# Kernel tuning notes

Hardware: AMD Instinct MI355X
Metric: run time of the kernel (lower is better)

## Reference

```python
import jax, jax.numpy as jnp
import numpy as np

N, E, IN, H, O, D = 1024, 65536, 768, 512, 256, 5
THRESH = 0.5
SAVE_W = [float(np.exp(0.0)), float(np.exp(-1.0)), float(np.exp(-2.0))]  # exp(-layers_pos)


def _gcn_conv(x, ei, ew, W, b):
    """PyG GCNConv: x@W, add self-loops (weight 1), symmetric degree norm, scatter-add."""
    n = x.shape[0]
    h = x @ W                                   # [n, out]
    loop = jnp.arange(n)
    src = jnp.concatenate([ei[0], loop])
    dst = jnp.concatenate([ei[1], loop])
    w = jnp.concatenate([ew, jnp.ones((n,), h.dtype)])
    deg = jax.ops.segment_sum(w, dst, num_segments=n)
    dinv = jnp.where(deg > 0, deg ** -0.5, 0.0)
    coef = dinv[src] * w * dinv[dst]
    return jax.ops.segment_sum(coef[:, None] * h[src], dst, num_segments=n) + b


def _spectral_flags(X):
    """Cosine-similarity graph -> unnormalized Laplacian -> eigengap-based class ids (int)."""
    Xn = X / (jnp.linalg.norm(X, axis=1, keepdims=True) + 1e-8)
    S = Xn @ Xn.T                               # [N, N]
    Lap = jnp.diag(S.sum(1)) - S
    ev = jax.lax.stop_gradient(jnp.linalg.eigvalsh(Lap))  # discrete downstream -> no grad
    order = jnp.argsort(ev)
    sv = ev[order]
    newc = (jnp.diff(sv) > THRESH).astype(jnp.int32)
    cls_sorted = jnp.concatenate([jnp.zeros((1,), jnp.int32), jnp.cumsum(newc)])
    return jnp.zeros((X.shape[0],), jnp.int32).at[order].set(cls_sorted)


def _class_avg(flags, X):
    """Per-class mean feature, gathered back to every node."""
    n = X.shape[0]
    sums = jax.ops.segment_sum(X, flags, num_segments=n)
    cnt = jax.ops.segment_sum(jnp.ones((n,), X.dtype), flags, num_segments=n)
    avg = sums / jnp.clip(cnt, 1.0)[:, None]
    return avg[flags]


def setup_inputs() -> dict:
    key = jax.random.key(0)
    ks = jax.random.split(key, 32)
    f32 = jnp.float32

    def p(k, shape, fan_in):
        return jax.random.normal(k, shape, f32) * (fan_in ** -0.5)

    inp = {}
    for i in range(5):
        inp[f'dim{i + 1}'] = jax.random.normal(ks[i], (N, IN), f32)
    inp['edge_indices'] = jax.random.randint(ks[5], (D, 2, E), 0, N)
    inp['edge_weights'] = jax.random.uniform(ks[6], (D, E), f32, 0.1, 1.0)
    inp['non_zero'] = jax.random.uniform(ks[7], (N,), f32, 1.0, 5.0)
    inp['gcn_w1'] = p(ks[8], (D, H, H), H)
    inp['gcn_b1'] = p(ks[9], (D, H), H)
    inp['gcn_w2'] = p(ks[10], (D, O, O), O)
    inp['gcn_b2'] = p(ks[11], (D, O), O)
    inp['gcn_w3'] = p(ks[12], (D, O, O), O)
    inp['gcn_b3'] = p(ks[13], (D, O), O)
    inp['gcn_wb'] = p(ks[14], (D, O, O), O)   # beh_conv1 (the only beh conv actually called)
    inp['gcn_bb'] = p(ks[15], (D, O), O)
    inp['w_pre1'] = p(ks[16], (IN, H), IN)
    inp['b_pre1'] = p(ks[17], (H,), IN)
    inp['w_pre2'] = p(ks[18], (H, O), H)
    inp['b_pre2'] = p(ks[19], (O,), H)
    inp['w_pre3'] = p(ks[20], (O, O), O)
    inp['b_pre3'] = p(ks[21], (O,), O)
    inp['w_beh1'] = p(ks[22], (O, O), O)
    inp['b_beh1'] = p(ks[23], (O,), O)
    inp['w_beh2'] = p(ks[24], (O, O), O)
    inp['b_beh2'] = p(ks[25], (O,), O)
    inp['w_beh3'] = p(ks[26], (O, O), O)
    inp['b_beh3'] = p(ks[27], (O,), O)
    inp['dim_weights'] = jnp.ones((D,), f32) + 0.1 * jax.random.normal(ks[28], (D,), f32)
    inp['k_save'] = jnp.asarray(0.5, f32)
    return inp


def reference(dim1, dim2, dim3, dim4, dim5, edge_indices, edge_weights, non_zero,
              gcn_w1, gcn_b1, gcn_w2, gcn_b2, gcn_w3, gcn_b3, gcn_wb, gcn_bb,
              w_pre1, b_pre1, w_pre2, b_pre2, w_pre3, b_pre3,
              w_beh1, b_beh1, w_beh2, b_beh2, w_beh3, b_beh3,
              dim_weights, k_save):
    dims = jnp.stack([dim1, dim2, dim3, dim4, dim5])      # [D, N, IN]
    dw = dim_weights / dim_weights.sum()
    gcn = jax.vmap(_gcn_conv)

    def pre_layer(x, Wl, bl, Wg, bg, save_w):
        lin = jnp.einsum('dni,io->dno', x, Wl) + bl       # shared Linear over all dims
        outs = gcn(lin, edge_indices, edge_weights, Wg, bg)
        fused = jnp.einsum('d,dnc->nc', dw, outs)         # weighted dimension fusion
        mg = lin + (save_w * fused / non_zero[:, None])[None]
        return jax.nn.relu(lin + mg)                      # relu(lin + (lin + upd))

    L1 = pre_layer(dims, w_pre1, b_pre1, gcn_w1, gcn_b1, SAVE_W[0])
    L2 = pre_layer(L1, w_pre2, b_pre2, gcn_w2, gcn_b2, SAVE_W[1])
    L3 = pre_layer(L2, w_pre3, b_pre3, gcn_w3, gcn_b3, SAVE_W[2])

    def beh_layer(g_in, fir, Wl, bl):
        g = gcn(g_in, edge_indices, edge_weights, gcn_wb, gcn_bb)  # always beh_conv1
        flags = jax.vmap(_spectral_flags)(g)
        avg = jax.vmap(_class_avg)(flags, g)
        lin = jnp.einsum('dni,io->dno', avg, Wl) + bl
        fea = fir + k_save * lin
        return g, jax.nn.relu(fir + fea)

    g4, L4 = beh_layer(L3, L3, w_beh1, b_beh1)
    g5, L5 = beh_layer(g4, L4, w_beh2, b_beh2)
    g6, L6 = beh_layer(g5, L5, w_beh3, b_beh3)
    return L6.sum(axis=0) + 1e-8                          # [N, O]
```

## Files before the change

### kernel.cpp

```cpp
#include <hip/hip_runtime.h>
#include <math.h>


#define NNODE 1024
#define NEDGE 65536
#define NDIM  5
#define TN    1024
#define TDW   48

struct P5 { const float* p[5]; };

__device__ __forceinline__ float wave_red_sum(float v) {
#pragma unroll
  for (int o = 32; o; o >>= 1) v += __shfl_xor(v, o);
  return v;
}

__global__ __launch_bounds__(256) void ws_fail_kernel(float* __restrict__ out, float val) {
  out[(size_t)blockIdx.x * 256 + threadIdx.x] = val;
}

__global__ __launch_bounds__(256) void count_edges_kernel(const int* __restrict__ eidx,
                                                          int* __restrict__ cnt) {
  long i = (long)blockIdx.x * 256 + threadIdx.x;
  if (i >= (long)NDIM * NEDGE) return;
  int d = (int)(i / NEDGE), e = (int)(i % NEDGE);
  int dst = eidx[(long)d * 2 * NEDGE + NEDGE + e];
  atomicAdd(&cnt[d * NNODE + dst], 1);
}

__global__ __launch_bounds__(1024) void scan_kernel(const int* __restrict__ cnt,
                                                    int* __restrict__ rowptr,
                                                    int* __restrict__ fillpos) {
  int d = blockIdx.x, i = threadIdx.x;
  __shared__ int s[1024];
  int c = cnt[d * NNODE + i];
  s[i] = c;
  __syncthreads();
  for (int off = 1; off < 1024; off <<= 1) {
    int t = (i >= off) ? s[i - off] : 0;
    __syncthreads();
    s[i] += t;
    __syncthreads();
  }
  int excl = s[i] - c;
  rowptr[d * (NNODE + 1) + i] = excl;
  fillpos[d * NNODE + i] = excl;
  if (i == 1023) rowptr[d * (NNODE + 1) + NNODE] = s[i];
}

__global__ __launch_bounds__(256) void csr_fill_kernel(const int* __restrict__ eidx,
                                                       int* __restrict__ fillpos,
                                                       int* __restrict__ csr) {
  long i = (long)blockIdx.x * 256 + threadIdx.x;
  if (i >= (long)NDIM * NEDGE) return;
  int d = (int)(i / NEDGE), e = (int)(i % NEDGE);
  int dst = eidx[(long)d * 2 * NEDGE + NEDGE + e];
  int pos = atomicAdd(&fillpos[d * NNODE + dst], 1);
  csr[(long)d * NEDGE + pos] = e;
}

__global__ __launch_bounds__(256) void csr_sort_kernel(const int* __restrict__ rowptr,
                                                       int* __restrict__ csr) {
  int idx = blockIdx.x * 256 + threadIdx.x;
  if (idx >= NDIM * NNODE) return;
  int d = idx >> 10, n = idx & 1023;
  int rs = rowptr[d * (NNODE + 1) + n], re = rowptr[d * (NNODE + 1) + n + 1];
  int* a = csr + (long)d * NEDGE;
  for (int i = rs + 1; i < re; ++i) {
    int key = a[i]; int j = i - 1;
    while (j >= rs && a[j] > key) { a[j + 1] = a[j]; --j; }
    a[j + 1] = key;
  }
}

__global__ __launch_bounds__(256) void deg_kernel(const int* __restrict__ rowptr,
                                                  const int* __restrict__ csr,
                                                  const float* __restrict__ ew,
                                                  float* __restrict__ dinv,
                                                  float* __restrict__ selfc) {
  int idx = blockIdx.x * 256 + threadIdx.x;
  if (idx >= NDIM * NNODE) return;
  int d = idx >> 10, n = idx & 1023;
  int rs = rowptr[d * (NNODE + 1) + n], re = rowptr[d * (NNODE + 1) + n + 1];
  const float* ewd = ew + (long)d * NEDGE;
  const int* csrd = csr + (long)d * NEDGE;
  float deg = 1.0f;
  for (int t = rs; t < re; ++t) deg += ewd[csrd[t]];
  float di = 1.0f / sqrtf(deg);
  dinv[idx] = di;
  selfc[idx] = di * di;
}

__global__ __launch_bounds__(256) void coef_kernel(const int* __restrict__ eidx,
                                                   const float* __restrict__ ew,
                                                   const float* __restrict__ dinv,
                                                   float* __restrict__ coef) {
  long i = (long)blockIdx.x * 256 + threadIdx.x;
  if (i >= (long)NDIM * NEDGE) return;
  int d = (int)(i / NEDGE), e = (int)(i % NEDGE);
  int s = eidx[(long)d * 2 * NEDGE + e];
  int t = eidx[(long)d * 2 * NEDGE + NEDGE + e];
  coef[i] = dinv[d * NNODE + s] * ew[i] * dinv[d * NNODE + t];
}

__global__ __launch_bounds__(256) void gemm_nn(P5 Ap, const float* __restrict__ B, long Bstr,
                                               const float* __restrict__ bias,
                                               float* __restrict__ C, long Cstr,
                                               int Nn, int K) {
  int z = blockIdx.z;
  const float* A = Ap.p[z];
  const float* Bz = B + (size_t)z * Bstr;
  float* Cz = C + (size_t)z * Cstr;
  __shared__ float As[16][65], Bs[16][65];
  int bx = blockIdx.x * 64, by = blockIdx.y * 64;
  int tid = threadIdx.x, tx = tid & 15, ty = tid >> 4;
  float acc[4][4] = {};
  for (int k0 = 0; k0 < K; k0 += 16) {
    {
      int r = tid >> 2, kk = (tid & 3) * 4;
      float4 v = *(const float4*)(A + (size_t)(by + r) * K + k0 + kk);
      As[kk + 0][r] = v.x; As[kk + 1][r] = v.y; As[kk + 2][r] = v.z; As[kk + 3][r] = v.w;
    }
    {
      int kk = tid >> 4, c4 = (tid & 15) * 4;
      float4 v = *(const float4*)(Bz + (size_t)(k0 + kk) * Nn + bx + c4);
      Bs[kk][c4 + 0] = v.x; Bs[kk][c4 + 1] = v.y; Bs[kk][c4 + 2] = v.z; Bs[kk][c4 + 3] = v.w;
    }
    __syncthreads();
#pragma unroll
    for (int kk = 0; kk < 16; ++kk) {
      float a[4], b[4];
#pragma unroll
      for (int u = 0; u < 4; ++u) { a[u] = As[kk][ty * 4 + u]; b[u] = Bs[kk][tx * 4 + u]; }
#pragma unroll
      for (int ii = 0; ii < 4; ++ii)
#pragma unroll
        for (int jj = 0; jj < 4; ++jj) acc[ii][jj] += a[ii] * b[jj];
    }
    __syncthreads();
  }
#pragma unroll
  for (int ii = 0; ii < 4; ++ii)
#pragma unroll
    for (int jj = 0; jj < 4; ++jj) {
      int gj = bx + tx * 4 + jj;
      float v = acc[ii][jj];
      if (bias) v += bias[gj];
      Cz[(size_t)(by + ty * 4 + ii) * Nn + gj] = v;
    }
}

__global__ __launch_bounds__(256) void gemm_nt_lap(const float* __restrict__ Xn,
                                                   const float* __restrict__ svec,
                                                   float* __restrict__ Lap) {
  int z = blockIdx.z;
  const float* X = Xn + (size_t)z * NNODE * 256;
  float* C = Lap + (size_t)z * NNODE * NNODE;
  __shared__ float As[16][65], Bs[16][65];
  int bx = blockIdx.x * 64, by = blockIdx.y * 64;
  int tid = threadIdx.x, tx = tid & 15, ty = tid >> 4;
  float acc[4][4] = {};
  for (int k0 = 0; k0 < 256; k0 += 16) {
    int r = tid >> 2, kk = (tid & 3) * 4;
    float4 va = *(const float4*)(X + (size_t)(by + r) * 256 + k0 + kk);
    As[kk + 0][r] = va.x; As[kk + 1][r] = va.y; As[kk + 2][r] = va.z; As[kk + 3][r] = va.w;
    float4 vb4 = *(const float4*)(X + (size_t)(bx + r) * 256 + k0 + kk);
    Bs[kk + 0][r] = vb4.x; Bs[kk + 1][r] = vb4.y; Bs[kk + 2][r] = vb4.z; Bs[kk + 3][r] = vb4.w;
    __syncthreads();
#pragma unroll
    for (int kk2 = 0; kk2 < 16; ++kk2) {
      float a[4], b[4];
#pragma unroll
      for (int u = 0; u < 4; ++u) { a[u] = As[kk2][ty * 4 + u]; b[u] = Bs[kk2][tx * 4 + u]; }
#pragma unroll
      for (int ii = 0; ii < 4; ++ii)
#pragma unroll
        for (int jj = 0; jj < 4; ++jj) acc[ii][jj] += a[ii] * b[jj];
    }
    __syncthreads();
  }
#pragma unroll
  for (int ii = 0; ii < 4; ++ii)
#pragma unroll
    for (int jj = 0; jj < 4; ++jj) {
      int gi = by + ty * 4 + ii, gj = bx + tx * 4 + jj;
      float v = -acc[ii][jj];
      if (gi == gj) v += svec[z * NNODE + gi];
      C[(size_t)gi * NNODE + gj] = v;
    }
}

__global__ __launch_bounds__(256) void gcn_gather(const float* __restrict__ h,
                                                  const int* __restrict__ eidx,
                                                  const int* __restrict__ csr,
                                                  const int* __restrict__ rowptr,
                                                  const float* __restrict__ coef,
                                                  const float* __restrict__ selfc,
                                                  const float* __restrict__ bg,
                                                  float* __restrict__ outp, int C) {
  int n = blockIdx.x, d = blockIdx.y;
  const float* hd = h + (size_t)d * NNODE * C;
  float* od = outp + (size_t)d * NNODE * C;
  const int* srcA = eidx + (size_t)d * 2 * NEDGE;
  const float* coefd = coef + (size_t)d * NEDGE;
  const int* csrd = csr + (size_t)d * NEDGE;
  int rs = rowptr[d * (NNODE + 1) + n], re = rowptr[d * (NNODE + 1) + n + 1];
  float sc = selfc[d * NNODE + n];
  for (int c = threadIdx.x; c < C; c += 256) {
    float acc = sc * hd[(size_t)n * C + c] + bg[d * C + c];
    for (int idx = rs; idx < re; ++idx) {
      int e = csrd[idx];
      acc += coefd[e] * hd[(size_t)srcA[e] * C + c];
    }
    od[(size_t)n * C + c] = acc;
  }
}

__global__ __launch_bounds__(256) void pre_fuse(const float* __restrict__ lin,
                                                const float* __restrict__ outs,
                                                const float* __restrict__ nz,
                                                const float* __restrict__ dimw,
                                                float saveW, float* __restrict__ Lout, int C) {
  size_t i = (size_t)blockIdx.x * 256 + threadIdx.x;
  int n = (int)(i / C);
  float s0 = dimw[0], s1 = dimw[1], s2 = dimw[2], s3 = dimw[3], s4 = dimw[4];
  float S = s0 + s1 + s2 + s3 + s4;
  size_t st = (size_t)NNODE * C;
  float fused = s0 * outs[i] + s1 * outs[i + st] + s2 * outs[i + 2 * st] +
                s3 * outs[i + 3 * st] + s4 * outs[i + 4 * st];
  float addv = saveW * fused / (S * nz[n]);
#pragma unroll
  for (int d = 0; d < 5; ++d) {
    float l = lin[i + d * st];
    Lout[i + d * st] = fmaxf(2.f * l + addv, 0.f);
  }
}

__global__ __launch_bounds__(256) void rownorm_kernel(const float* __restrict__ g,
                                                      float* __restrict__ Xn) {
  int n = blockIdx.x, d = blockIdx.y, t = threadIdx.x;
  __shared__ float red[4];
  size_t base = ((size_t)d * NNODE + n) * 256;
  float v = g[base + t];
  float sq = wave_red_sum(v * v);
  if ((t & 63) == 0) red[t >> 6] = sq;
  __syncthreads();
  float ss = red[0] + red[1] + red[2] + red[3];
  float inv = 1.f / (sqrtf(ss) + 1e-8f);
  Xn[base + t] = v * inv;
}

__global__ __launch_bounds__(256) void colsum_kernel(const float* __restrict__ Xn,
                                                     float* __restrict__ tcol) {
  int d = blockIdx.y, c = threadIdx.x;
  float acc = 0.f;
  const float* p = Xn + (size_t)d * NNODE * 256 + c;
  for (int i = 0; i < NNODE; ++i) acc += p[(size_t)i * 256];
  tcol[d * 256 + c] = acc;
}

__global__ __launch_bounds__(256) void sdot_kernel(const float* __restrict__ Xn,
                                                   const float* __restrict__ tcol,
                                                   float* __restrict__ svec) {
  int n = blockIdx.x, d = blockIdx.y, t = threadIdx.x;
  __shared__ float red[4];
  size_t base = ((size_t)d * NNODE + n) * 256;
  float v = wave_red_sum(Xn[base + t] * tcol[d * 256 + t]);
  if ((t & 63) == 0) red[t >> 6] = v;
  __syncthreads();
  if (t == 0) svec[d * NNODE + n] = red[0] + red[1] + red[2] + red[3];
}

__global__ __launch_bounds__(256) void col_init_kernel(const float* __restrict__ Lap,
                                                       float* __restrict__ colbufG) {
  int i = blockIdx.x * 256 + threadIdx.x;
  int d = blockIdx.y;
  colbufG[(size_t)d * TN + i] = Lap[(size_t)d * TN * TN + (size_t)i * TN + 0];
}

__global__ __launch_bounds__(256) void tristep(float* __restrict__ Amats,
                                               float* __restrict__ colbufG,
                                               float* __restrict__ prawG,
                                               float* __restrict__ vglobG,
                                               float* __restrict__ tauG,
                                               float* __restrict__ dT,
                                               float* __restrict__ eT,
                                               int k) {
  const int mat = blockIdx.x % NDIM;
  const int wgl = blockIdx.x / NDIM;
  const int WGM = gridDim.x / NDIM;
  const int WPM = WGM * 4;
  const int tid = threadIdx.x;
  const int lane = tid & 63;
  const int wid = tid >> 6;
  const int wv = wgl * 4 + wid;

  float* A = Amats + (size_t)mat * TN * TN;
  const int s0 = k & 1, s1 = (k + 1) & 1;
  const float* colA = colbufG + ((size_t)s0 * NDIM + mat) * TN;
  float* colB = colbufG + ((size_t)s1 * NDIM + mat) * TN;
  const float* prawP = prawG + ((size_t)s1 * NDIM + mat) * TN;
  float* prawC = prawG + ((size_t)s0 * NDIM + mat) * TN;
  const float* vprevG = vglobG + ((size_t)s1 * NDIM + mat) * TN;
  float* vcurG = vglobG + ((size_t)s0 * NDIM + mat) * TN;

  __shared__ float vprev[TN], vcur[TN], wb[TN];
  __shared__ float redA[4], redK[4];

  float tau_prev = (k > 0) ? tauG[s1 * NDIM + mat] : 0.f;

  float kp = 0.f;
  for (int j = k + tid; j < TN; j += 256) {
    float v = (k > 0) ? vprevG[j] : 0.f;
    vprev[j] = v;
    kp += (k > 0) ? v * prawP[j] : 0.f;
  }
  kp = wave_red_sum(kp);
  if (lane == 0) redK[wid] = kp;
  __syncthreads();
  float Kraw = redK[0] + redK[1] + redK[2] + redK[3];
  float c2p = 0.5f * tau_prev * tau_prev * Kraw;
  for (int j = k + tid; j < TN; j += 256)
    wb[j] = (k > 0) ? (tau_prev * prawP[j] - c2p * vprev[j]) : 0.f;
  __syncthreads();

  float wkk = wb[k];
  float vkk = vprev[k];
  float sp = 0.f;
  for (int i = k + 1 + tid; i < TN; i += 256) {
    float c = colA[i] - vprev[i] * wkk - wb[i] * vkk;
    vcur[i] = c;
    sp += c * c;
  }
  sp = wave_red_sum(sp);
  if (lane == 0) redA[wid] = sp;
  __syncthreads();
  float sigma = redA[0] + redA[1] + redA[2] + redA[3];

  if (wgl == 0 && tid == 0)
    dT[mat * TN + k] = A[(size_t)k * TN + k] - 2.f * vkk * wkk;

  float c0 = vcur[k + 1];
  float alpha, tau;
  if (sigma < 1e-30f) { alpha = 0.f; tau = 0.f; }
  else {
    alpha = (c0 >= 0.f) ? -sqrtf(sigma) : sqrtf(sigma);
    tau = 2.f / (2.f * alpha * (alpha - c0));
  }
  __syncthreads();
  if (tid == 0) vcur[k + 1] = c0 - alpha;
  if (wgl == 0 && tid == 0) { eT[mat * TN + k] = alpha; tauG[s0 * NDIM + mat] = tau; }
  __syncthreads();

  if (wgl == 0)
    for (int j = k + 1 + tid; j < TN; j += 256) vcurG[j] = vcur[j];

  int i0 = (k + 1) + ((wv - ((k + 1) % WPM) + WPM) % WPM);
  for (int i = i0; i < TN; i += WPM) {
    float vi = vprev[i];
    float wi = wb[i];
    float* row = A + (size_t)i * TN;
    float dot = 0.f;
    if (k > 0) {
      for (int j = k + 1 + lane; j < TN; j += 64) {
        float a = row[j] - vi * wb[j] - wi * vprev[j];
        row[j] = a;
        dot += a * vcur[j];
        if (j == k + 1) colB[i] = a;
      }
    } else {
      for (int j = 1 + lane; j < TN; j += 64) {
        float a = row[j];
        dot += a * vcur[j];
        if (j == 1) colB[i] = a;
      }
    }
    dot = wave_red_sum(dot);
    if (lane == 0) prawC[i] = dot;
  }
}

__global__ __launch_bounds__(64) void tritail(const float* __restrict__ Amats,
                                              const float* __restrict__ prawG,
                                              const float* __restrict__ vglobG,
                                              const float* __restrict__ tauG,
                                              float* __restrict__ dT,
                                              float* __restrict__ eT) {
  int mat = threadIdx.x;
  if (mat >= NDIM) return;
  const int k = TN - 3;
  const int s0 = k & 1;
  const float* v = vglobG + ((size_t)s0 * NDIM + mat) * TN;
  const float* pr = prawG + ((size_t)s0 * NDIM + mat) * TN;
  float tau = tauG[s0 * NDIM + mat];
  const float* A = Amats + (size_t)mat * TN * TN;
  const int i1 = TN - 2, i2 = TN - 1;
  float v1 = v[i1], v2 = v[i2];
  float Kraw = v1 * pr[i1] + v2 * pr[i2];
  float c2 = 0.5f * tau * tau * Kraw;
  float w1 = tau * pr[i1] - c2 * v1;
  float w2 = tau * pr[i2] - c2 * v2;
  float a11 = A[(size_t)i1 * TN + i1];
  float a21 = A[(size_t)i2 * TN + i1];
  float a22 = A[(size_t)i2 * TN + i2];
  dT[mat * TN + i1] = a11 - 2.f * v1 * w1;
  eT[mat * TN + i1] = a21 - v2 * w1 - w2 * v1;
  dT[mat * TN + i2] = a22 - 2.f * v2 * w2;
}

__global__ __launch_bounds__(256) void bisect_kernel(const float* __restrict__ dT,
                                                     const float* __restrict__ eT,
                                                     float* __restrict__ ev) {
  int mat = blockIdx.y;
  int i = blockIdx.x * 256 + threadIdx.x;
  __shared__ float ds[TN], es[TN];
  __shared__ float redmn[4], redmx[4];
  for (int t = threadIdx.x; t < TN; t += 256) {
    ds[t] = dT[mat * TN + t];
    es[t] = (t < TN - 1) ? eT[mat * TN + t] : 0.f;
  }
  __syncthreads();
  float mn = 1e30f, mx = -1e30f;
  for (int t = threadIdx.x; t < TN; t += 256) {
    float ep = (t > 0) ? fabsf(es[t - 1]) : 0.f;
    float r = ep + fabsf(es[t]);
    mn = fminf(mn, ds[t] - r);
    mx = fmaxf(mx, ds[t] + r);
  }
#pragma unroll
  for (int o = 32; o; o >>= 1) {
    mn = fminf(mn, __shfl_xor(mn, o));
    mx = fmaxf(mx, __shfl_xor(mx, o));
  }
  if ((threadIdx.x & 63) == 0) { redmn[threadIdx.x >> 6] = mn; redmx[threadIdx.x >> 6] = mx; }
  __syncthreads();
  mn = fminf(fminf(redmn[0], redmn[1]), fminf(redmn[2], redmn[3]));
  mx = fmaxf(fmaxf(redmx[0], redmx[1]), fmaxf(redmx[2], redmx[3]));
  float pad = 1e-3f + 1e-6f * fmaxf(fabsf(mn), fabsf(mx));
  float lo = mn - pad, hi = mx + pad;
  const float PIV = 1e-12f;
  for (int it = 0; it < 40; ++it) {
    float x = 0.5f * (lo + hi);
    if (!(x > lo && x < hi)) break;
    float q = ds[0] - x;
    if (fabsf(q) < PIV) q = -PIV;
    int cntv = (q < 0.f) ? 1 : 0;
    for (int t = 1; t < TN; ++t) {
      float e = es[t - 1];
      q = (ds[t] - x) - __fdividef(e * e, q);
      if (fabsf(q) < PIV) q = -PIV;
      cntv += (q < 0.f) ? 1 : 0;
    }
    if (cntv <= i) lo = x; else hi = x;
  }
  ev[mat * TN + i] = 0.5f * (lo + hi);
}

__global__ __launch_bounds__(1024) void flags_kernel(const float* __restrict__ ev,
                                                     int* __restrict__ flags,
                                                     int* __restrict__ startI,
                                                     int* __restrict__ ncls) {
  int d = blockIdx.x, i = threadIdx.x;
  __shared__ int s[1024];
  float evi = ev[d * TN + i];
  int g = 0;
  if (i < TN - 1) g = ((ev[d * TN + i + 1] - evi) > 0.5f) ? 1 : 0;
  s[i] = g;
  __syncthreads();
  for (int off = 1; off < 1024; off <<= 1) {
    int t = (i >= off) ? s[i - off] : 0;
    __syncthreads();
    s[i] += t;
    __syncthreads();
  }
  int fl = s[i] - g;
  flags[d * TN + i] = fl;
  if (i == 0) startI[d * (TN + 1)] = 0;
  if (i < TN - 1 && g) startI[d * (TN + 1) + fl + 1] = i + 1;
  if (i == TN - 1) { ncls[d] = fl + 1; startI[d * (TN + 1) + fl + 1] = TN; }
}

__global__ __launch_bounds__(256) void class_avg_kernel(const float* __restrict__ g,
                                                        const int* __restrict__ startI,
                                                        const int* __restrict__ ncls,
                                                        float* __restrict__ avg) {
  int c = blockIdx.x, d = blockIdx.y, t = threadIdx.x;
  size_t base = (size_t)d * NNODE * 256;
  float* o = avg + base + (size_t)c * 256 + t;
  if (c >= ncls[d]) { *o = 0.f; return; }
  int rs = startI[d * (NNODE + 1) + c], re = startI[d * (NNODE + 1) + c + 1];
  float acc = 0.f;
  for (int r = rs; r < re; ++r) acc += g[base + (size_t)r * 256 + t];
  *o = acc / (float)(re - rs);
}

__global__ __launch_bounds__(256) void beh_out_kernel(const float* __restrict__ fir,
                                                      const float* __restrict__ linB,
                                                      const int* __restrict__ flags,
                                                      const float* __restrict__ ksave,
                                                      float* __restrict__ Lout) {
  size_t i = (size_t)blockIdx.x * 256 + threadIdx.x;
  int c = (int)(i & 255);
  int n = (int)((i >> 8) & 1023);
  int d = (int)(i >> 18);
  float k = ksave[0];
  int f = flags[d * NNODE + n];
  float lv = linB[((size_t)d * NNODE + f) * 256 + c];
  Lout[i] = fmaxf(2.f * fir[i] + k * lv, 0.f);
}

__global__ __launch_bounds__(256) void final_sum_kernel(const float* __restrict__ L6,
                                                        float* __restrict__ out) {
  size_t i = (size_t)blockIdx.x * 256 + threadIdx.x;
  size_t st = (size_t)NNODE * 256;
  out[i] = L6[i] + L6[i + st] + L6[i + 2 * st] + L6[i + 3 * st] + L6[i + 4 * st] + 1e-8f;
}

extern "C" void kernel_launch(void* const* d_in, const int* in_sizes, int n_in,
                              void* d_out, int out_size, void* d_ws, size_t ws_size,
                              hipStream_t stream) {
  (void)in_sizes; (void)n_in; (void)out_size;
  const float* dimp[5];
  for (int i = 0; i < 5; ++i) dimp[i] = (const float*)d_in[i];
  const int* eidx = (const int*)d_in[5];
  const float* ew = (const float*)d_in[6];
  const float* nz = (const float*)d_in[7];
  const float* gw1 = (const float*)d_in[8];
  const float* gb1 = (const float*)d_in[9];
  const float* gw2 = (const float*)d_in[10];
  const float* gb2 = (const float*)d_in[11];
  const float* gw3 = (const float*)d_in[12];
  const float* gb3 = (const float*)d_in[13];
  const float* gwb = (const float*)d_in[14];
  const float* gbb = (const float*)d_in[15];
  const float* wp1 = (const float*)d_in[16];
  const float* bp1 = (const float*)d_in[17];
  const float* wp2 = (const float*)d_in[18];
  const float* bp2 = (const float*)d_in[19];
  const float* wp3 = (const float*)d_in[20];
  const float* bp3 = (const float*)d_in[21];
  const float* wb1 = (const float*)d_in[22];
  const float* bb1 = (const float*)d_in[23];
  const float* wb2 = (const float*)d_in[24];
  const float* bb2 = (const float*)d_in[25];
  const float* wb3 = (const float*)d_in[26];
  const float* bb3 = (const float*)d_in[27];
  const float* dimw = (const float*)d_in[28];
  const float* ksave = (const float*)d_in[29];
  float* out = (float*)d_out;

  char* wsb = (char*)d_ws;
  size_t off = 0;
  auto alloc = [&](size_t bytes) -> char* {
    char* p = wsb + off;
    off = (off + bytes + 255) & ~(size_t)255;
    return p;
  };
  float* Lap = (float*)alloc((size_t)NDIM * TN * TN * 4);
  float* lin = Lap;
  float* outs = Lap + (size_t)NDIM * NNODE * 512;
  float* hbuf = (float*)alloc((size_t)NDIM * NNODE * 512 * 4);
  float* L1 = (float*)alloc((size_t)NDIM * NNODE * 512 * 4);
  float* L2 = (float*)alloc((size_t)NDIM * NNODE * 256 * 4);
  float* L3 = (float*)alloc((size_t)NDIM * NNODE * 256 * 4);
  float* gA = (float*)alloc((size_t)NDIM * NNODE * 256 * 4);
  float* gB = (float*)alloc((size_t)NDIM * NNODE * 256 * 4);
  float* dinv = (float*)alloc((size_t)NDIM * NNODE * 4);
  float* selfc = (float*)alloc((size_t)NDIM * NNODE * 4);
  int* cnt = (int*)alloc((size_t)NDIM * NNODE * 4);
  int* rowptr = (int*)alloc((size_t)NDIM * (NNODE + 1) * 4);
  int* fillpos = (int*)alloc((size_t)NDIM * NNODE * 4);
  int* csr = (int*)alloc((size_t)NDIM * NEDGE * 4);
  float* coef = (float*)alloc((size_t)NDIM * NEDGE * 4);
  float* tcol = (float*)alloc((size_t)NDIM * 256 * 4);
  float* svec = (float*)alloc((size_t)NDIM * NNODE * 4);
  float* colbufG = (float*)alloc((size_t)2 * NDIM * TN * 4);
  float* prawG = (float*)alloc((size_t)2 * NDIM * TN * 4);
  float* vglobG = (float*)alloc((size_t)2 * NDIM * TN * 4);
  float* tauG = (float*)alloc((size_t)2 * NDIM * 4);
  float* dT = (float*)alloc((size_t)NDIM * NNODE * 4);
  float* eT = (float*)alloc((size_t)NDIM * NNODE * 4);
  float* ev = (float*)alloc((size_t)NDIM * NNODE * 4);
  int* flags = (int*)alloc((size_t)NDIM * NNODE * 4);
  int* startI = (int*)alloc((size_t)NDIM * (NNODE + 1) * 4);
  int* nclsI = (int*)alloc(256);

  if (off > ws_size) {
    ws_fail_kernel<<<dim3(1024), dim3(256), 0, stream>>>(
        out, 1.0e6f + (float)(ws_size >> 20));
    return;
  }

  float* L4 = L1;
  float* L5 = L2;
  float* L6 = L3;
  float* Xn = hbuf;
  float* avgbuf = outs;
  float* linB = lin;

  hipMemsetAsync(cnt, 0, (size_t)NDIM * NNODE * 4, stream);

  dim3 B256(256);
  count_edges_kernel<<<dim3((NDIM * NEDGE) / 256), B256, 0, stream>>>(eidx, cnt);
  scan_kernel<<<dim3(NDIM), dim3(1024), 0, stream>>>(cnt, rowptr, fillpos);
  csr_fill_kernel<<<dim3((NDIM * NEDGE) / 256), B256, 0, stream>>>(eidx, fillpos, csr);
  csr_sort_kernel<<<dim3(20), B256, 0, stream>>>(rowptr, csr);
  deg_kernel<<<dim3(20), B256, 0, stream>>>(rowptr, csr, ew, dinv, selfc);
  coef_kernel<<<dim3((NDIM * NEDGE) / 256), B256, 0, stream>>>(eidx, ew, dinv, coef);

  auto mk5 = [](const float* base, size_t stride) {
    P5 s;
    for (int z = 0; z < 5; ++z) s.p[z] = base + z * stride;
    return s;
  };

  P5 x1; for (int z = 0; z < 5; ++z) x1.p[z] = dimp[z];
  gemm_nn<<<dim3(8, 16, 5), B256, 0, stream>>>(x1, wp1, 0, bp1, lin, (long)NNODE * 512, 512, 768);
  gemm_nn<<<dim3(8, 16, 5), B256, 0, stream>>>(mk5(lin, (size_t)NNODE * 512), gw1, (long)512 * 512,
                                               nullptr, hbuf, (long)NNODE * 512, 512, 512);
  gcn_gather<<<dim3(NNODE, NDIM), B256, 0, stream>>>(hbuf, eidx, csr, rowptr, coef, selfc, gb1, outs, 512);
  pre_fuse<<<dim3(2048), B256, 0, stream>>>(lin, outs, nz, dimw, 1.0f, L1, 512);

  gemm_nn<<<dim3(4, 16, 5), B256, 0, stream>>>(mk5(L1, (size_t)NNODE * 512), wp2, 0, bp2, lin,
                                               (long)NNODE * 256, 256, 512);
  gemm_nn<<<dim3(4, 16, 5), B256, 0, stream>>>(mk5(lin, (size_t)NNODE * 256), gw2, (long)256 * 256,
                                               nullptr, hbuf, (long)NNODE * 256, 256, 256);
  gcn_gather<<<dim3(NNODE, NDIM), B256, 0, stream>>>(hbuf, eidx, csr, rowptr, coef, selfc, gb2, outs, 256);
  pre_fuse<<<dim3(1024), B256, 0, stream>>>(lin, outs, nz, dimw, 0.36787944117144233f, L2, 256);

  gemm_nn<<<dim3(4, 16, 5), B256, 0, stream>>>(mk5(L2, (size_t)NNODE * 256), wp3, 0, bp3, lin,
                                               (long)NNODE * 256, 256, 256);
  gemm_nn<<<dim3(4, 16, 5), B256, 0, stream>>>(mk5(lin, (size_t)NNODE * 256), gw3, (long)256 * 256,
                                               nullptr, hbuf, (long)NNODE * 256, 256, 256);
  gcn_gather<<<dim3(NNODE, NDIM), B256, 0, stream>>>(hbuf, eidx, csr, rowptr, coef, selfc, gb3, outs, 256);
  pre_fuse<<<dim3(1024), B256, 0, stream>>>(lin, outs, nz, dimw, 0.13533528323661270f, L3, 256);

  auto beh = [&](const float* g_in, const float* fir, const float* Wl, const float* bl,
                 float* g_out, float* Lout) {
    gemm_nn<<<dim3(4, 16, 5), B256, 0, stream>>>(mk5(g_in, (size_t)NNODE * 256), gwb, (long)256 * 256,
                                                 nullptr, hbuf, (long)NNODE * 256, 256, 256);
    gcn_gather<<<dim3(NNODE, NDIM), B256, 0, stream>>>(hbuf, eidx, csr, rowptr, coef, selfc, gbb, g_out, 256);
    rownorm_kernel<<<dim3(NNODE, NDIM), B256, 0, stream>>>(g_out, Xn);
    colsum_kernel<<<dim3(1, NDIM), B256, 0, stream>>>(Xn, tcol);
    sdot_kernel<<<dim3(NNODE, NDIM), B256, 0, stream>>>(Xn, tcol, svec);
    gemm_nt_lap<<<dim3(16, 16, 5), B256, 0, stream>>>(Xn, svec, Lap);
    col_init_kernel<<<dim3(4, NDIM), B256, 0, stream>>>(Lap, colbufG);
    for (int k = 0; k <= TN - 3; ++k)
      tristep<<<dim3(NDIM * TDW), B256, 0, stream>>>(Lap, colbufG, prawG, vglobG, tauG, dT, eT, k);
    tritail<<<dim3(1), dim3(64), 0, stream>>>(Lap, prawG, vglobG, tauG, dT, eT);
    bisect_kernel<<<dim3(4, NDIM), B256, 0, stream>>>(dT, eT, ev);
    flags_kernel<<<dim3(NDIM), dim3(1024), 0, stream>>>(ev, flags, startI, nclsI);
    class_avg_kernel<<<dim3(NNODE, NDIM), B256, 0, stream>>>(g_out, startI, nclsI, avgbuf);
    gemm_nn<<<dim3(4, 16, 5), B256, 0, stream>>>(mk5(avgbuf, (size_t)NNODE * 256), Wl, 0, bl, linB,
                                                 (long)NNODE * 256, 256, 256);
    beh_out_kernel<<<dim3(5120), B256, 0, stream>>>(fir, linB, flags, ksave, Lout);
  };
  beh(L3, L3, wb1, bb1, gA, L4);
  beh(gA, L4, wb2, bb2, gB, L5);
  beh(gB, L5, wb3, bb3, gA, L6);

  final_sum_kernel<<<dim3(1024), B256, 0, stream>>>(L6, out);
}
```

Measured before the change: 44.00 ms.

## Batch all three behaviour-layer eigen tridiagonalizations into one 15-matrix pass

The graph-conv chain for the three behaviour layers does not depend on the layer outputs, so all three conv results are computed first. Their fifteen Laplacians are then tridiagonalized together in a single sequence of ~1022 tristep launches, instead of three sequences over five matrices each. This targets the serial per-step launch overhead that dominates the eigen solve. In exchange it needs a larger workspace, spreads fewer workgroups over each matrix (16 instead of 48), and keeps a fallback to the old path when the workspace is too small.

New measurement: 38.48 ms. -12.5%, faster.

```diff
diff --git a/kernel.cpp b/kernel.cpp
--- a/kernel.cpp
+++ b/kernel.cpp
@@ -6,7 +6,9 @@
 #define NEDGE 65536
 #define NDIM  5
 #define TN    1024
+#define NMATS 15
 #define TDW   48
+#define TDWM  16
 
 struct P5 { const float* p[5]; };
 
@@ -286,10 +288,10 @@
                                                float* __restrict__ tauG,
                                                float* __restrict__ dT,
                                                float* __restrict__ eT,
-                                               int k) {
-  const int mat = blockIdx.x % NDIM;
-  const int wgl = blockIdx.x / NDIM;
-  const int WGM = gridDim.x / NDIM;
+                                               int nm, int k) {
+  const int mat = blockIdx.x % nm;
+  const int wgl = blockIdx.x / nm;
+  const int WGM = gridDim.x / nm;
   const int WPM = WGM * 4;
   const int tid = threadIdx.x;
   const int lane = tid & 63;
@@ -298,17 +300,17 @@
 
   float* A = Amats + (size_t)mat * TN * TN;
   const int s0 = k & 1, s1 = (k + 1) & 1;
-  const float* colA = colbufG + ((size_t)s0 * NDIM + mat) * TN;
-  float* colB = colbufG + ((size_t)s1 * NDIM + mat) * TN;
-  const float* prawP = prawG + ((size_t)s1 * NDIM + mat) * TN;
-  float* prawC = prawG + ((size_t)s0 * NDIM + mat) * TN;
-  const float* vprevG = vglobG + ((size_t)s1 * NDIM + mat) * TN;
-  float* vcurG = vglobG + ((size_t)s0 * NDIM + mat) * TN;
+  const float* colA = colbufG + ((size_t)s0 * nm + mat) * TN;
+  float* colB = colbufG + ((size_t)s1 * nm + mat) * TN;
+  const float* prawP = prawG + ((size_t)s1 * nm + mat) * TN;
+  float* prawC = prawG + ((size_t)s0 * nm + mat) * TN;
+  const float* vprevG = vglobG + ((size_t)s1 * nm + mat) * TN;
+  float* vcurG = vglobG + ((size_t)s0 * nm + mat) * TN;
 
   __shared__ float vprev[TN], vcur[TN], wb[TN];
   __shared__ float redA[4], redK[4];
 
-  float tau_prev = (k > 0) ? tauG[s1 * NDIM + mat] : 0.f;
+  float tau_prev = (k > 0) ? tauG[s1 * nm + mat] : 0.f;
 
   float kp = 0.f;
   for (int j = k + tid; j < TN; j += 256) {
@@ -350,7 +352,7 @@
   }
   __syncthreads();
   if (tid == 0) vcur[k + 1] = c0 - alpha;
-  if (wgl == 0 && tid == 0) { eT[mat * TN + k] = alpha; tauG[s0 * NDIM + mat] = tau; }
+  if (wgl == 0 && tid == 0) { eT[mat * TN + k] = alpha; tauG[s0 * nm + mat] = tau; }
   __syncthreads();
 
   if (wgl == 0)
@@ -386,14 +388,15 @@
                                               const float* __restrict__ vglobG,
                                               const float* __restrict__ tauG,
                                               float* __restrict__ dT,
-                                              float* __restrict__ eT) {
+                                              float* __restrict__ eT,
+                                              int nm) {
   int mat = threadIdx.x;
-  if (mat >= NDIM) return;
+  if (mat >= nm) return;
   const int k = TN - 3;
   const int s0 = k & 1;
-  const float* v = vglobG + ((size_t)s0 * NDIM + mat) * TN;
-  const float* pr = prawG + ((size_t)s0 * NDIM + mat) * TN;
-  float tau = tauG[s0 * NDIM + mat];
+  const float* v = vglobG + ((size_t)s0 * nm + mat) * TN;
+  const float* pr = prawG + ((size_t)s0 * nm + mat) * TN;
+  float tau = tauG[s0 * nm + mat];
   const float* A = Amats + (size_t)mat * TN * TN;
   const int i1 = TN - 2, i2 = TN - 1;
   float v1 = v[i1], v2 = v[i2];
@@ -551,53 +554,70 @@
   float* out = (float*)d_out;
 
   char* wsb = (char*)d_ws;
+  const size_t S512 = (size_t)NDIM * NNODE * 512;
+  const size_t S256 = (size_t)NDIM * NNODE * 256;
+
+  float *big, *lin, *outs, *hbuf, *L1, *L2, *L3, *gA, *gB, *gC, *XnE;
+  float *Lap, *L4, *L5, *L6, *avgbuf, *linB;
+  float *dinv, *selfc, *coef, *tcol, *svec, *colbufG, *prawG, *vglobG, *tauG, *dT, *eT, *ev;
+  int *cnt, *rowptr, *fillpos, *csr, *flags, *startI, *nclsI;
+
   size_t off = 0;
-  auto alloc = [&](size_t bytes) -> char* {
+  auto al = [&](size_t bytes) -> char* {
     char* p = wsb + off;
     off = (off + bytes + 255) & ~(size_t)255;
     return p;
   };
-  float* Lap = (float*)alloc((size_t)NDIM * TN * TN * 4);
-  float* lin = Lap;
-  float* outs = Lap + (size_t)NDIM * NNODE * 512;
-  float* hbuf = (float*)alloc((size_t)NDIM * NNODE * 512 * 4);
-  float* L1 = (float*)alloc((size_t)NDIM * NNODE * 512 * 4);
-  float* L2 = (float*)alloc((size_t)NDIM * NNODE * 256 * 4);
-  float* L3 = (float*)alloc((size_t)NDIM * NNODE * 256 * 4);
-  float* gA = (float*)alloc((size_t)NDIM * NNODE * 256 * 4);
-  float* gB = (float*)alloc((size_t)NDIM * NNODE * 256 * 4);
-  float* dinv = (float*)alloc((size_t)NDIM * NNODE * 4);
-  float* selfc = (float*)alloc((size_t)NDIM * NNODE * 4);
-  int* cnt = (int*)alloc((size_t)NDIM * NNODE * 4);
-  int* rowptr = (int*)alloc((size_t)NDIM * (NNODE + 1) * 4);
-  int* fillpos = (int*)alloc((size_t)NDIM * NNODE * 4);
-  int* csr = (int*)alloc((size_t)NDIM * NEDGE * 4);
-  float* coef = (float*)alloc((size_t)NDIM * NEDGE * 4);
-  float* tcol = (float*)alloc((size_t)NDIM * 256 * 4);
-  float* svec = (float*)alloc((size_t)NDIM * NNODE * 4);
-  float* colbufG = (float*)alloc((size_t)2 * NDIM * TN * 4);
-  float* prawG = (float*)alloc((size_t)2 * NDIM * TN * 4);
-  float* vglobG = (float*)alloc((size_t)2 * NDIM * TN * 4);
-  float* tauG = (float*)alloc((size_t)2 * NDIM * 4);
-  float* dT = (float*)alloc((size_t)NDIM * NNODE * 4);
-  float* eT = (float*)alloc((size_t)NDIM * NNODE * 4);
-  float* ev = (float*)alloc((size_t)NDIM * NNODE * 4);
-  int* flags = (int*)alloc((size_t)NDIM * NNODE * 4);
-  int* startI = (int*)alloc((size_t)NDIM * (NNODE + 1) * 4);
-  int* nclsI = (int*)alloc(256);
-
-  if (off > ws_size) {
-    ws_fail_kernel<<<dim3(1024), dim3(256), 0, stream>>>(
-        out, 1.0e6f + (float)(ws_size >> 20));
-    return;
-  }
-
-  float* L4 = L1;
-  float* L5 = L2;
-  float* L6 = L3;
-  float* Xn = hbuf;
-  float* avgbuf = outs;
-  float* linB = lin;
+  auto build = [&](bool merged) -> size_t {
+    off = 0;
+    size_t bigN = merged ? (size_t)NMATS * TN * TN
+                         : (4 * S512 + S256);
+    big = (float*)al(bigN * 4);
+    lin = big; outs = lin + S512; hbuf = outs + S512; L1 = hbuf + S512; L2 = L1 + S512;
+    L3 = (float*)al(S256 * 4);
+    gA = (float*)al(S256 * 4);
+    gB = (float*)al(S256 * 4);
+    if (merged) { gC = (float*)al(S256 * 4); XnE = (float*)al(S256 * 4); }
+    else        { gC = gA;                   XnE = hbuf; }
+    Lap = big;
+    if (merged) {
+      L4 = big; L5 = big + S256; L6 = big + 2 * S256;
+      avgbuf = big + 3 * S256; linB = big + 4 * S256;
+    } else {
+      L4 = L1; L5 = L1 + S256; L6 = L2;
+      avgbuf = outs; linB = lin;
+    }
+    dinv = (float*)al((size_t)NDIM * NNODE * 4);
+    selfc = (float*)al((size_t)NDIM * NNODE * 4);
+    cnt = (int*)al((size_t)NDIM * NNODE * 4);
+    rowptr = (int*)al((size_t)NDIM * (NNODE + 1) * 4);
+    fillpos = (int*)al((size_t)NDIM * NNODE * 4);
+    csr = (int*)al((size_t)NDIM * NEDGE * 4);
+    coef = (float*)al((size_t)NDIM * NEDGE * 4);
+    tcol = (float*)al((size_t)NDIM * 256 * 4);
+    svec = (float*)al((size_t)NDIM * NNODE * 4);
+    colbufG = (float*)al((size_t)2 * NMATS * TN * 4);
+    prawG = (float*)al((size_t)2 * NMATS * TN * 4);
+    vglobG = (float*)al((size_t)2 * NMATS * TN * 4);
+    tauG = (float*)al((size_t)2 * NMATS * 4);
+    dT = (float*)al((size_t)NMATS * TN * 4);
+    eT = (float*)al((size_t)NMATS * TN * 4);
+    ev = (float*)al((size_t)NMATS * TN * 4);
+    flags = (int*)al((size_t)NMATS * TN * 4);
+    startI = (int*)al((size_t)NMATS * (TN + 1) * 4);
+    nclsI = (int*)al(256);
+    return off;
+  };
+
+  bool merged = true;
+  if (build(true) > ws_size) {
+    merged = false;
+    if (build(false) > ws_size) {
+      ws_fail_kernel<<<dim3(1024), dim3(256), 0, stream>>>(
+          out, 1.0e6f + (float)(ws_size >> 20));
+      return;
+    }
+  }
 
   hipMemsetAsync(cnt, 0, (size_t)NDIM * NNODE * 4, stream);
 
@@ -636,29 +656,59 @@
   gcn_gather<<<dim3(NNODE, NDIM), B256, 0, stream>>>(hbuf, eidx, csr, rowptr, coef, selfc, gb3, outs, 256);
   pre_fuse<<<dim3(1024), B256, 0, stream>>>(lin, outs, nz, dimw, 0.13533528323661270f, L3, 256);
 
-  auto beh = [&](const float* g_in, const float* fir, const float* Wl, const float* bl,
-                 float* g_out, float* Lout) {
-    gemm_nn<<<dim3(4, 16, 5), B256, 0, stream>>>(mk5(g_in, (size_t)NNODE * 256), gwb, (long)256 * 256,
+  auto gconv = [&](const float* src, float* dst) {
+    gemm_nn<<<dim3(4, 16, 5), B256, 0, stream>>>(mk5(src, (size_t)NNODE * 256), gwb, (long)256 * 256,
                                                  nullptr, hbuf, (long)NNODE * 256, 256, 256);
-    gcn_gather<<<dim3(NNODE, NDIM), B256, 0, stream>>>(hbuf, eidx, csr, rowptr, coef, selfc, gbb, g_out, 256);
-    rownorm_kernel<<<dim3(NNODE, NDIM), B256, 0, stream>>>(g_out, Xn);
-    colsum_kernel<<<dim3(1, NDIM), B256, 0, stream>>>(Xn, tcol);
-    sdot_kernel<<<dim3(NNODE, NDIM), B256, 0, stream>>>(Xn, tcol, svec);
-    gemm_nt_lap<<<dim3(16, 16, 5), B256, 0, stream>>>(Xn, svec, Lap);
-    col_init_kernel<<<dim3(4, NDIM), B256, 0, stream>>>(Lap, colbufG);
-    for (int k = 0; k <= TN - 3; ++k)
-      tristep<<<dim3(NDIM * TDW), B256, 0, stream>>>(Lap, colbufG, prawG, vglobG, tauG, dT, eT, k);
-    tritail<<<dim3(1), dim3(64), 0, stream>>>(Lap, prawG, vglobG, tauG, dT, eT);
-    bisect_kernel<<<dim3(4, NDIM), B256, 0, stream>>>(dT, eT, ev);
-    flags_kernel<<<dim3(NDIM), dim3(1024), 0, stream>>>(ev, flags, startI, nclsI);
-    class_avg_kernel<<<dim3(NNODE, NDIM), B256, 0, stream>>>(g_out, startI, nclsI, avgbuf);
+    gcn_gather<<<dim3(NNODE, NDIM), B256, 0, stream>>>(hbuf, eidx, csr, rowptr, coef, selfc, gbb, dst, 256);
+  };
+  auto laplacian = [&](const float* g, float* LapDst) {
+    rownorm_kernel<<<dim3(NNODE, NDIM), B256, 0, stream>>>(g, XnE);
+    colsum_kernel<<<dim3(1, NDIM), B256, 0, stream>>>(XnE, tcol);
+    sdot_kernel<<<dim3(NNODE, NDIM), B256, 0, stream>>>(XnE, tcol, svec);
+    gemm_nt_lap<<<dim3(16, 16, 5), B256, 0, stream>>>(XnE, svec, LapDst);
+  };
+  auto lchain = [&](const float* g, const float* fir, const float* Wl, const float* bl,
+                    int slot, float* Lout) {
+    class_avg_kernel<<<dim3(NNODE, NDIM), B256, 0, stream>>>(
+        g, startI + slot * 5 * (NNODE + 1), nclsI + slot * 5, avgbuf);
     gemm_nn<<<dim3(4, 16, 5), B256, 0, stream>>>(mk5(avgbuf, (size_t)NNODE * 256), Wl, 0, bl, linB,
                                                  (long)NNODE * 256, 256, 256);
-    beh_out_kernel<<<dim3(5120), B256, 0, stream>>>(fir, linB, flags, ksave, Lout);
+    beh_out_kernel<<<dim3(5120), B256, 0, stream>>>(fir, linB, flags + slot * 5 * NNODE, ksave, Lout);
   };
-  beh(L3, L3, wb1, bb1, gA, L4);
-  beh(gA, L4, wb2, bb2, gB, L5);
-  beh(gB, L5, wb3, bb3, gA, L6);
-
-  final_sum_kernel<<<dim3(1024), B256, 0, stream>>>(L6, out);
-}
+
+  if (merged) {
+    gconv(L3, gA); gconv(gA, gB); gconv(gB, gC);
+    laplacian(gA, Lap);
+    laplacian(gB, Lap + (size_t)5 * TN * TN);
+    laplacian(gC, Lap + (size_t)10 * TN * TN);
+    col_init_kernel<<<dim3(4, NMATS), B256, 0, stream>>>(Lap, colbufG);
+    for (int k = 0; k <= TN - 3; ++k)
+      tristep<<<dim3(NMATS * TDWM), B256, 0, stream>>>(Lap, colbufG, prawG, vglobG, tauG, dT, eT,
+                                                       NMATS, k);
+    tritail<<<dim3(1), dim3(64), 0, stream>>>(Lap, prawG, vglobG, tauG, dT, eT, NMATS);
+    bisect_kernel<<<dim3(4, NMATS), B256, 0, stream>>>(dT, eT, ev);
+    flags_kernel<<<dim3(NMATS), dim3(1024), 0, stream>>>(ev, flags, startI, nclsI);
+    lchain(gA, L3, wb1, bb1, 0, L4);
+    lchain(gB, L4, wb2, bb2, 1, L5);
+    lchain(gC, L5, wb3, bb3, 2, L6);
+    final_sum_kernel<<<dim3(1024), B256, 0, stream>>>(L6, out);
+  } else {
+    auto beh = [&](const float* g_in, const float* fir, const float* Wl, const float* bl,
+                   float* g_out, float* Lout) {
+      gconv(g_in, g_out);
+      laplacian(g_out, Lap);
+      col_init_kernel<<<dim3(4, NDIM), B256, 0, stream>>>(Lap, colbufG);
+      for (int k = 0; k <= TN - 3; ++k)
+        tristep<<<dim3(NDIM * TDW), B256, 0, stream>>>(Lap, colbufG, prawG, vglobG, tauG, dT, eT,
+                                                       NDIM, k);
+      tritail<<<dim3(1), dim3(64), 0, stream>>>(Lap, prawG, vglobG, tauG, dT, eT, NDIM);
+      bisect_kernel<<<dim3(4, NDIM), B256, 0, stream>>>(dT, eT, ev);
+      flags_kernel<<<dim3(NDIM), dim3(1024), 0, stream>>>(ev, flags, startI, nclsI);
+      lchain(g_out, fir, Wl, bl, 0, Lout);
+    };
+    beh(L3, L3, wb1, bb1, gA, L4);
+    beh(gA, L4, wb2, bb2, gB, L5);
+    beh(gB, L5, wb3, bb3, gA, L6);
+    final_sum_kernel<<<dim3(1024), B256, 0, stream>>>(L6, out);
+  }
+}
```
